# Optimization experiments

Measured on AMD Instinct MI355X. Metric: run time of the kernel, lower is better.

Reference implementation:

```python
import jax, jax.numpy as jnp
import numpy as np

B, S, D, H, W1, G = 2, 4096, 768, 12, 256, 8  # W1 = one-sided window (attention_window // 2)
HD = D // H
NC = S // W1  # number of query chunks of size W1
NEG = -1e9


def setup_inputs():
    key = jax.random.key(0)
    ks = jax.random.split(key, 9)
    def w(k):
        return jax.random.normal(k, (D, D), jnp.float32) * 0.02
    zb = jnp.zeros((D,), jnp.float32)
    # mask: >0 global, 0 local, <0 masked. First G tokens are global.
    mask = jnp.zeros((B, 1, 1, S), jnp.int32).at[:, :, :, :G].set(1)
    return {
        "hidden_states": jax.random.normal(ks[0], (B, S, D), jnp.float32),
        "attention_mask": mask,
        "Wq": w(ks[1]), "bq": zb,
        "Wk": w(ks[2]), "bk": zb,
        "Wv": w(ks[3]), "bv": zb,
        "Wqg": w(ks[4]), "bqg": zb,
        "Wkg": w(ks[5]), "bkg": zb,
        "Wvg": w(ks[6]), "bvg": zb,
        "Wo": w(ks[7]), "bo": zb,
        "n_global": G,
    }


def reference(hidden_states, attention_mask, Wq, bq, Wk, bk, Wv, bv,
              Wqg, bqg, Wkg, bkg, Wvg, bvg, Wo, bo, n_global):
    g = n_global
    mask = attention_mask.reshape(B, S)
    key_neg = mask < 0  # masked-out positions
    scale = 1.0 / np.sqrt(HD)

    def heads(x):  # [B,S,D] -> [B,H,S,HD]
        return x.reshape(B, S, H, HD).transpose(0, 2, 1, 3)

    q = heads(hidden_states @ Wq + bq) * scale
    k = heads(hidden_states @ Wk + bk)
    v = heads(hidden_states @ Wv + bv)

    # ---- sliding-window (banded) scores via 3-chunk gather ----
    idx = jnp.arange(NC)[:, None] * W1 + jnp.arange(3 * W1)[None, :]  # [NC,3W] into padded seq
    k_ch = jnp.pad(k, ((0, 0), (0, 0), (W1, W1), (0, 0)))[:, :, idx]  # [B,H,NC,3W,HD]
    q_ch = q.reshape(B, H, NC, W1, HD)
    band = jnp.einsum('bhcqd,bhckd->bhcqk', q_ch, k_ch)  # [B,H,NC,W,3W]

    qi = jnp.arange(W1)
    kj = jnp.arange(3 * W1)
    band_ok = jnp.abs(kj[None, :] - W1 - qi[:, None]) <= W1        # [W,3W] |j-i|<=w
    j_abs = idx - W1                                               # absolute key index
    in_range = (j_abs >= 0) & (j_abs < S)                          # [NC,3W]
    neg_ch = jnp.pad(key_neg, ((0, 0), (W1, W1)))[:, idx]          # [B,NC,3W]
    valid = (band_ok[None, None, None]
             & in_range[None, None, :, None, :]
             & (~neg_ch)[:, None, :, None, :])                     # [B,1,NC,W,3W]
    band = jnp.where(valid, band, NEG)

    # ---- scores of every query against the global keys (regular k proj) ----
    glob = jnp.einsum('bhsd,bhgd->bhsg', q, k[:, :, :g])           # [B,H,S,G]
    glob = jnp.where(key_neg[:, None, None, :g], NEG, glob)

    scores = jnp.concatenate([glob.reshape(B, H, NC, W1, g), band], axis=-1)
    probs = jax.nn.softmax(scores, axis=-1)
    probs = jnp.where(key_neg.reshape(B, 1, NC, W1, 1), 0.0, probs)  # zero masked query rows

    v_ch = jnp.pad(v, ((0, 0), (0, 0), (W1, W1), (0, 0)))[:, :, idx]
    out = jnp.einsum('bhcqk,bhckd->bhcqd', probs[..., g:], v_ch)
    out = out + jnp.einsum('bhcqg,bhgd->bhcqd', probs[..., :g], v[:, :, :g])
    out = out.reshape(B, H, S, HD)

    # ---- global tokens: full attention with dedicated global projections ----
    qg = heads(hidden_states @ Wqg + bqg)[:, :, :g] * scale        # [B,H,G,HD]
    kg = heads(hidden_states @ Wkg + bkg)
    vg = heads(hidden_states @ Wvg + bvg)
    gs = jnp.einsum('bhgd,bhsd->bhgs', qg, kg)                     # [B,H,G,S]
    gs = jnp.where(key_neg[:, None, None, :], NEG, gs)
    gp = jax.nn.softmax(gs, axis=-1)
    og = jnp.einsum('bhgs,bhsd->bhgd', gp, vg)
    out = out.at[:, :, :g].set(og)

    merged = out.transpose(0, 2, 1, 3).reshape(B, S, D)
    return merged @ Wo + bo  # outer output projection
```

## Files before the change

### kernel.cpp

```cpp
#include <hip/hip_runtime.h>

#define BB 2
#define SS 4096
#define DD 768
#define HH 12
#define HDD 64
#define W1C 256
#define NCC 16
#define GG 8

typedef unsigned short u16;
typedef __attribute__((ext_vector_type(4))) unsigned short u16x4;
typedef __attribute__((ext_vector_type(8))) unsigned short u16x8;
typedef __attribute__((ext_vector_type(8))) short s16x8;
typedef __attribute__((ext_vector_type(4))) float f32x4;

__device__ __forceinline__ float b2f(u16 u) {
  union { unsigned int i; float f; } v;
  v.i = ((unsigned int)u) << 16;
  return v.f;
}
__device__ __forceinline__ u16 f2b(float f) {
  union { float f; unsigned int i; } v;
  v.f = f;
  unsigned int r = v.i + 0x7FFFu + ((v.i >> 16) & 1u);
  return (u16)(r >> 16);
}
__device__ __forceinline__ float fexp2(float x) {
#if __has_builtin(__builtin_amdgcn_exp2f)
  return __builtin_amdgcn_exp2f(x);
#else
  return exp2f(x);
#endif
}
__device__ __forceinline__ unsigned pk_bf16(float lo, float hi) {
  unsigned r;
  asm("v_cvt_pk_bf16_f32 %0, %1, %2" : "=v"(r) : "v"(lo), "v"(hi));
  return r;
}
__device__ __forceinline__ void load_lds16(const void* g, void* l) {
  __builtin_amdgcn_global_load_lds(
      (const __attribute__((address_space(1))) unsigned int*)g,
      (__attribute__((address_space(3))) unsigned int*)l, 16, 0, 0);
}

#define QSCALE 0.18033688011112042f

struct WtArgs { const float* W[6]; };

__global__ __launch_bounds__(256) void prep(
    const float* __restrict__ hs, WtArgs wa, const float* __restrict__ Wqg,
    const float* __restrict__ bqg, u16* __restrict__ Ab,
    u16* __restrict__ WT, u16* __restrict__ QG) {
  __shared__ __align__(16) char pshm[24576];
  const int bid = blockIdx.x;
  const int t = threadIdx.x;

  if (bid < 3072) {
    int i = bid * 256 + t;
    const float4* p = (const float4*)(hs + (size_t)i * 8);
    float4 a = p[0], b = p[1];
    u16x8 o;
    o[0] = f2b(a.x); o[1] = f2b(a.y); o[2] = f2b(a.z); o[3] = f2b(a.w);
    o[4] = f2b(b.x); o[5] = f2b(b.y); o[6] = f2b(b.z); o[7] = f2b(b.w);
    *(u16x8*)(Ab + (size_t)i * 8) = o;
  } else if (bid < 3936) {
    float (*T)[65] = (float (*)[65])pshm;
    const int t2 = bid - 3072;
    const int mat = t2 / 144;
    const int rem = t2 % 144;
    const int k0 = (rem / 12) * 64;
    const int n0 = (rem % 12) * 64;
    const float* __restrict__ W = wa.W[mat];
#pragma unroll
    for (int i = 0; i < 4; i++) {
      int idx4 = t + i * 256;
      int r = idx4 >> 4, c4 = idx4 & 15;
      float4 v = *(const float4*)(W + (size_t)(k0 + r) * 768 + n0 + c4 * 4);
      T[r][c4 * 4 + 0] = v.x; T[r][c4 * 4 + 1] = v.y;
      T[r][c4 * 4 + 2] = v.z; T[r][c4 * 4 + 3] = v.w;
    }
    __syncthreads();
#pragma unroll
    for (int i = 0; i < 2; i++) {
      int ci = t + i * 256;
      int nl = ci >> 3, k8 = ci & 7;
      u16x8 o;
#pragma unroll
      for (int jj = 0; jj < 8; jj++) o[jj] = f2b(T[k8 * 8 + jj][nl]);
      *(u16x8*)(WT + ((size_t)mat * 768 + n0 + nl) * 768 + k0 + k8 * 8) = o;
    }
  } else {
    float (*hsL)[768] = (float (*)[768])pshm;
    const int bh = bid - 3936;
    const int b = bh / HH, h = bh % HH;
#pragma unroll
    for (int i = 0; i < 6; i++) {
      int idx = t + i * 256;
      int row = idx / 192, c4 = idx % 192;
      *(float4*)&hsL[row][c4 * 4] =
          *(const float4*)(hs + ((size_t)b * SS + row) * DD + c4 * 4);
    }
    __syncthreads();
#pragma unroll
    for (int rep = 0; rep < 2; rep++) {
      int qi = rep * 4 + (t >> 6);
      int d = t & 63, n = h * 64 + d;
      float acc = bqg[n];
      for (int k = 0; k < DD; k++)
        acc = fmaf(hsL[qi][k], Wqg[(size_t)k * DD + n], acc);
      QG[((size_t)bh * 16 + qi) * 64 + d] = f2b(acc * QSCALE);
    }
#pragma unroll
    for (int i = 0; i < 2; i++) {
      int idx = t + i * 256;
      int row = 8 + (idx >> 6), d = idx & 63;
      QG[((size_t)bh * 16 + row) * 64 + d] = 0;
    }
  }
}

struct BiasArgs { const float* bias[5]; };

template <int MODE>
__global__ __launch_bounds__(512, 1) void gemm_bf16(
    const u16* __restrict__ A, const u16* __restrict__ WT, BiasArgs ba,
    u16* __restrict__ outb, float* __restrict__ outf) {
  constexpr int NTL = (MODE == 0) ? 15 : 3;
  constexpr int NWG = 64 * NTL;
  constexpr int NT = 12;
  constexpr int ABYTES = 128 * 64 * 2;
  constexpr int BBYTES = 256 * 64 * 2;
  constexpr int BUFB = ABYTES + BBYTES;

  extern __shared__ __align__(16) char smem[];

  const int tid = threadIdx.x;
  const int w = tid >> 6, l = tid & 63;
  const int lq = l & 15, g = l >> 4;
  const int wm = w >> 2, wn = w & 3;

  const int cpx = NWG >> 3;
  const int id = (int)blockIdx.x;
  const int swz = (id & 7) * cpx + (id >> 3);
  const int bm = swz / NTL, bn = swz % NTL;
  const int m0 = bm * 128;
  const int nw0 = bn * 256;
  const int wsel = (MODE == 0) ? (bn / 3) : 0;
  const int nmat0 = (MODE == 0) ? ((bn % 3) * 256) : (bn * 256);
  const float* __restrict__ bias = ba.bias[wsel];

  f32x4 acc[4][4];
#pragma unroll
  for (int i = 0; i < 4; i++)
#pragma unroll
    for (int j = 0; j < 4; j++) acc[i][j] = (f32x4){0.f, 0.f, 0.f, 0.f};

  auto stage = [&](int t) {
    const int k0 = t * 64;
    char* uA = smem + (t % 3) * BUFB;
    char* uB = uA + ABYTES;
#pragma unroll
    for (int j = 0; j < 2; j++) {
      const int ci = j * 8 + w;
      const int p = ci * 64 + l;
      const int row = p >> 3, sl = p & 7;
      load_lds16(A + (size_t)(m0 + row) * 768 + k0 + ((sl ^ (row & 7)) * 8),
                 uA + ci * 1024);
    }
#pragma unroll
    for (int j = 0; j < 4; j++) {
      const int ci = j * 8 + w;
      const int p = ci * 64 + l;
      const int row = p >> 3, sl = p & 7;
      load_lds16(WT + (size_t)(nw0 + row) * 768 + k0 + ((sl ^ (row & 7)) * 8),
                 uB + ci * 1024);
    }
  };

  stage(0);
  stage(1);
  asm volatile("s_waitcnt vmcnt(6)" ::: "memory");
  __builtin_amdgcn_sched_barrier(0);
  __builtin_amdgcn_s_barrier();
  __builtin_amdgcn_sched_barrier(0);

  for (int kt = 0; kt < NT; kt++) {
    const u16* rA = (const u16*)(smem + (kt % 3) * BUFB);
    const u16* rB = (const u16*)(smem + (kt % 3) * BUFB + ABYTES);

    if (kt < NT - 2) stage(kt + 2);
    __builtin_amdgcn_sched_barrier(0);

    s16x8 af[4][2], bf[4][2];
#pragma unroll
    for (int mi = 0; mi < 4; mi++) {
      const int r = wm * 64 + mi * 16 + lq;
#pragma unroll
      for (int ks = 0; ks < 2; ks++)
        af[mi][ks] =
            *(const s16x8*)(rA + r * 64 + (((ks * 4 + g) ^ (r & 7)) * 8));
    }
#pragma unroll
    for (int nj = 0; nj < 4; nj++) {
      const int r = wn * 64 + nj * 16 + lq;
#pragma unroll
      for (int ks = 0; ks < 2; ks++)
        bf[nj][ks] =
            *(const s16x8*)(rB + r * 64 + (((ks * 4 + g) ^ (r & 7)) * 8));
    }
#pragma unroll
    for (int mi = 0; mi < 4; mi++)
#pragma unroll
      for (int nj = 0; nj < 4; nj++)
#pragma unroll
        for (int ks = 0; ks < 2; ks++)
          acc[mi][nj] = __builtin_amdgcn_mfma_f32_16x16x32_bf16(
              af[mi][ks], bf[nj][ks], acc[mi][nj], 0, 0, 0);

    if (kt < NT - 2)
      asm volatile("s_waitcnt vmcnt(6)" ::: "memory");
    else
      asm volatile("s_waitcnt vmcnt(0)" ::: "memory");
    __builtin_amdgcn_sched_barrier(0);
    __builtin_amdgcn_s_barrier();
    __builtin_amdgcn_sched_barrier(0);
  }

  if (MODE == 0) {
    const float scale = (wsel == 0) ? QSCALE : 1.0f;
    u16* outw = outb + (size_t)wsel * ((size_t)BB * HH * SS * HDD);
#pragma unroll
    for (int nj = 0; nj < 4; nj++) {
      const int c = nmat0 + wn * 64 + nj * 16 + lq;
      const float bv = bias[c];
      const int h = c >> 6, hd = c & 63;
#pragma unroll
      for (int mi = 0; mi < 4; mi++) {
#pragma unroll
        for (int r = 0; r < 4; r++) {
          const int m = m0 + wm * 64 + mi * 16 + g * 4 + r;
          const int b = m >> 12, s = m & 4095;
          outw[((size_t)(b * HH + h) * SS + s) * HDD + hd] =
              f2b((acc[mi][nj][r] + bv) * scale);
        }
      }
    }
  } else {
#pragma unroll
    for (int nj = 0; nj < 4; nj++) {
      const int c = nmat0 + wn * 64 + nj * 16 + lq;
      const float bv = bias[c];
#pragma unroll
      for (int mi = 0; mi < 4; mi++) {
#pragma unroll
        for (int r = 0; r < 4; r++) {
          const int m = m0 + wm * 64 + mi * 16 + g * 4 + r;
          outf[(size_t)m * 768 + c] = acc[mi][nj][r] + bv;
        }
      }
    }
  }
}

__global__ __launch_bounds__(512, 4) void attn_band(
    const u16* __restrict__ Q, const u16* __restrict__ K,
    const u16* __restrict__ V, const int* __restrict__ amask,
    u16* __restrict__ ATT) {
  __shared__ __align__(16) char smem[32768];
  const int tid = threadIdx.x;
  const int w = tid >> 6, lane = tid & 63;
  const int lq = lane & 15, g = lane >> 4;
  const int h = blockIdx.y, b = blockIdx.z;
  const int bh = b * HH + h;
  const size_t bhs = (size_t)bh * SS;
  const int q0 = (int)blockIdx.x * 128;

  s16x8 qf[2];
  {
    const u16* qp = Q + (bhs + q0 + w * 16 + lq) * 64;
    qf[0] = *(const s16x8*)(qp + g * 8);
    qf[1] = *(const s16x8*)(qp + 32 + g * 8);
  }

  f32x4 oacc[4];
#pragma unroll
  for (int i = 0; i < 4; i++) oacc[i] = (f32x4){0.f, 0.f, 0.f, 0.f};
  float denom = 0.f;

  const int NT = 11;
  u16x8 vreg;

  auto jof = [&](int t) { return t < 10 ? q0 - 256 + t * 64 : 0; };

  auto stage_issue = [&](int t) {
    const int j0 = jof(t);
    char* Kb_ = smem + (t & 1) * 16384;
    const int row = tid >> 3, sl = tid & 7;
    if (j0 >= 0 && j0 + 64 <= SS) {
      load_lds16(K + (bhs + j0 + row) * 64 + ((sl ^ (row & 7)) * 8),
                 Kb_ + w * 1024);
    } else {
      int jj = j0 + row;
      u16x8 val;
#pragma unroll
      for (int e = 0; e < 8; e++) val[e] = 0;
      if ((unsigned)jj < (unsigned)SS)
        val = *(const u16x8*)(K + (bhs + jj) * 64 + ((sl ^ (row & 7)) * 8));
      *(u16x8*)(Kb_ + tid * 16) = val;
    }
    int jj = j0 + lane;
    u16x8 vv;
#pragma unroll
    for (int e = 0; e < 8; e++) vv[e] = 0;
    if ((unsigned)jj < (unsigned)SS)
      vv = *(const u16x8*)(V + (bhs + jj) * 64 + w * 8);
    vreg = vv;
  };

  stage_issue(0);

  for (int kt = 0; kt < NT; kt++) {
    const int j0 = jof(kt);
    const int cur = kt & 1;
    char* Kl = smem + cur * 16384;
    char* VT = Kl + 8192;
    const bool bandfree = (kt == 10);
    const int klimit = bandfree ? 8 : 64;

    int jm = j0 + lane;
    int mv = ((unsigned)jm < (unsigned)SS) ? amask[b * SS + jm] : -1;
    bool okk = (mv >= 0) && (lane < klimit);
    unsigned long long vm = __ballot(okk);

    asm volatile("s_waitcnt vmcnt(0)" ::: "memory");
#pragma unroll
    for (int e = 0; e < 8; e++)
      *(u16*)(VT + (w * 8 + e) * 128 + ((lane * 2) ^ (e << 4))) = vreg[e];
    asm volatile("s_waitcnt lgkmcnt(0)" ::: "memory");
    __builtin_amdgcn_sched_barrier(0);
    __builtin_amdgcn_s_barrier();
    __builtin_amdgcn_sched_barrier(0);

    if (kt + 1 < NT) stage_issue(kt + 1);

    f32x4 sc[4];
#pragma unroll
    for (int i = 0; i < 4; i++) sc[i] = (f32x4){0.f, 0.f, 0.f, 0.f};
#pragma unroll
    for (int s = 0; s < 2; s++) {
#pragma unroll
      for (int ks = 0; ks < 4; ks++) {
        s16x8 kf = *(const s16x8*)(Kl + (ks * 16 + lq) * 128 +
                                   (((s * 4 + g) ^ (lq & 7)) << 4));
        sc[ks] = __builtin_amdgcn_mfma_f32_16x16x32_bf16(kf, qf[s], sc[ks],
                                                          0, 0, 0);
      }
    }

    {
      const unsigned mlo = (unsigned)vm, mhi = (unsigned)(vm >> 32);
      const int q_abs = q0 + w * 16 + lq;
      const int qw = q0 + w * 16;
      const bool allin = bandfree || (j0 >= qw - 241 && j0 <= qw + 193);
      const bool fast = (vm == ~0ull) && allin;
      const int ddq = j0 + g * 4 - q_abs;
      const int gsh = g * 4;
      if (fast) {
#pragma unroll
        for (int ks = 0; ks < 4; ks++)
#pragma unroll
          for (int r = 0; r < 4; r++) {
            float p = fexp2(sc[ks][r]);
            sc[ks][r] = p;
            denom += p;
          }
      } else {
#pragma unroll
        for (int ks = 0; ks < 4; ks++)
#pragma unroll
          for (int r = 0; r < 4; r++) {
            float e = fexp2(sc[ks][r]);
            unsigned bit =
                ((ks < 2 ? mlo : mhi) >> (gsh + ((ks & 1) * 16 + r))) & 1u;
            bool ok = bit && (allin ||
                              (unsigned)(ddq + ks * 16 + r + 256) <= 512u);
            float p = ok ? e : 0.f;
            sc[ks][r] = p;
            denom += p;
          }
      }
    }

#pragma unroll
    for (int s = 0; s < 2; s++) {
      const int srcA = lq + ((g & 1) << 5);
      const bool hiSel = g >= 2;
      float L[4], H[4];
#pragma unroll
      for (int r = 0; r < 4; r++) {
        float a0 = __shfl(sc[2 * s][r], srcA);
        float a1 = __shfl(sc[2 * s + 1][r], srcA);
        L[r] = hiSel ? a1 : a0;
        float b0 = __shfl(sc[2 * s][r], srcA + 16);
        float b1 = __shfl(sc[2 * s + 1][r], srcA + 16);
        H[r] = hiSel ? b1 : b0;
      }
      union { unsigned u[4]; s16x8 v; } pf;
      pf.u[0] = pk_bf16(L[0], L[1]);
      pf.u[1] = pk_bf16(L[2], L[3]);
      pf.u[2] = pk_bf16(H[0], H[1]);
      pf.u[3] = pk_bf16(H[2], H[3]);
#pragma unroll
      for (int dblk = 0; dblk < 4; dblk++) {
        s16x8 vf = *(const s16x8*)(VT + (dblk * 16 + lq) * 128 +
                                   (((s * 4 + g) ^ (lq & 7)) << 4));
        oacc[dblk] = __builtin_amdgcn_mfma_f32_16x16x32_bf16(vf, pf.v,
                                                              oacc[dblk],
                                                              0, 0, 0);
      }
    }

    __builtin_amdgcn_sched_barrier(0);
    __builtin_amdgcn_s_barrier();
    __builtin_amdgcn_sched_barrier(0);
  }

  denom += __shfl_xor(denom, 16);
  denom += __shfl_xor(denom, 32);
  const int q_abs = q0 + w * 16 + lq;
  const float rowscale = (amask[b * SS + q_abs] >= 0) ? (1.f / denom) : 0.f;
  u16* orow = ATT + ((size_t)b * SS + q_abs) * DD + h * 64;
#pragma unroll
  for (int dblk = 0; dblk < 4; dblk++) {
    u16x4 o;
#pragma unroll
    for (int r = 0; r < 4; r++) o[r] = f2b(oacc[dblk][r] * rowscale);
    *(u16x4*)(orow + dblk * 16 + g * 4) = o;
  }
}

__global__ __launch_bounds__(256) void attn_global(
    const u16* __restrict__ Q, const u16* __restrict__ K,
    const u16* __restrict__ V, const int* __restrict__ amask,
    float* __restrict__ Pnum, float* __restrict__ Pden) {
  extern __shared__ __align__(16) char smem[];
  const int tid = threadIdx.x;
  const int w = tid >> 6, lane = tid & 63;
  const int lq = lane & 15, g = lane >> 4;
  const int h = blockIdx.y, b = blockIdx.z;
  const int bh = b * HH + h;
  const size_t bhs = (size_t)bh * SS;
  const int split = (int)blockIdx.x;

  char* Kl = smem + w * 16384;
  char* VT = Kl + 8192;

  s16x8 qf[2];
  {
    const u16* qp = Q + ((size_t)bh * 16 + lq) * 64;
    qf[0] = *(const s16x8*)(qp + g * 8);
    qf[1] = *(const s16x8*)(qp + 32 + g * 8);
  }

  f32x4 oacc[4];
#pragma unroll
  for (int i = 0; i < 4; i++) oacc[i] = (f32x4){0.f, 0.f, 0.f, 0.f};
  float denom = 0.f;

  for (int kt = 0; kt < 2; kt++) {
    const int j0 = split * 512 + (w * 2 + kt) * 64;

    int jm = j0 + lane;
    int mv = amask[b * SS + jm];
    unsigned long long vm = __ballot(mv >= 0);

    asm volatile("s_waitcnt lgkmcnt(0)" ::: "memory");
    const u16* Ks = K + bhs * 64 + (size_t)j0 * 64;
#pragma unroll
    for (int i = 0; i < 8; i++) {
      int ci = i * 64 + lane;
      int row = ci >> 3, cc = ci & 7, cs = cc ^ (row & 7);
      load_lds16(Ks + row * 64 + cs * 8, Kl + i * 1024);
    }
    const u16* Vs = V + bhs * 64 + (size_t)j0 * 64;
#pragma unroll
    for (int p = 0; p < 8; p++) {
      u16x8 vv = *(const u16x8*)(Vs + (size_t)lane * 64 + p * 8);
#pragma unroll
      for (int e = 0; e < 8; e++)
        *(u16*)(VT + (p * 8 + e) * 128 + ((lane * 2) ^ (e << 4))) = vv[e];
    }
    asm volatile("s_waitcnt vmcnt(0) lgkmcnt(0)" ::: "memory");

    f32x4 sc[4];
#pragma unroll
    for (int i = 0; i < 4; i++) sc[i] = (f32x4){0.f, 0.f, 0.f, 0.f};
#pragma unroll
    for (int s = 0; s < 2; s++) {
#pragma unroll
      for (int ks = 0; ks < 4; ks++) {
        s16x8 kf = *(const s16x8*)(Kl + (ks * 16 + lq) * 128 +
                                   (((s * 4 + g) ^ (lq & 7)) << 4));
        sc[ks] = __builtin_amdgcn_mfma_f32_16x16x32_bf16(kf, qf[s], sc[ks],
                                                          0, 0, 0);
      }
    }

    {
      const unsigned mlo = (unsigned)vm, mhi = (unsigned)(vm >> 32);
      const bool fast = (vm == ~0ull);
      const int gsh = g * 4;
      if (fast) {
#pragma unroll
        for (int ks = 0; ks < 4; ks++)
#pragma unroll
          for (int r = 0; r < 4; r++) {
            float p = fexp2(sc[ks][r]);
            sc[ks][r] = p;
            denom += p;
          }
      } else {
#pragma unroll
        for (int ks = 0; ks < 4; ks++)
#pragma unroll
          for (int r = 0; r < 4; r++) {
            float e = fexp2(sc[ks][r]);
            unsigned bit =
                ((ks < 2 ? mlo : mhi) >> (gsh + ((ks & 1) * 16 + r))) & 1u;
            float p = bit ? e : 0.f;
            sc[ks][r] = p;
            denom += p;
          }
      }
    }

#pragma unroll
    for (int s = 0; s < 2; s++) {
      const int srcA = lq + ((g & 1) << 5);
      const bool hiSel = g >= 2;
      float L[4], H[4];
#pragma unroll
      for (int r = 0; r < 4; r++) {
        float a0 = __shfl(sc[2 * s][r], srcA);
        float a1 = __shfl(sc[2 * s + 1][r], srcA);
        L[r] = hiSel ? a1 : a0;
        float b0 = __shfl(sc[2 * s][r], srcA + 16);
        float b1 = __shfl(sc[2 * s + 1][r], srcA + 16);
        H[r] = hiSel ? b1 : b0;
      }
      union { unsigned u[4]; s16x8 v; } pf;
      pf.u[0] = pk_bf16(L[0], L[1]);
      pf.u[1] = pk_bf16(L[2], L[3]);
      pf.u[2] = pk_bf16(H[0], H[1]);
      pf.u[3] = pk_bf16(H[2], H[3]);
#pragma unroll
      for (int dblk = 0; dblk < 4; dblk++) {
        s16x8 vf = *(const s16x8*)(VT + (dblk * 16 + lq) * 128 +
                                   (((s * 4 + g) ^ (lq & 7)) << 4));
        oacc[dblk] = __builtin_amdgcn_mfma_f32_16x16x32_bf16(vf, pf.v,
                                                              oacc[dblk],
                                                              0, 0, 0);
      }
    }
  }

  denom += __shfl_xor(denom, 16);
  denom += __shfl_xor(denom, 32);
  const int pidx = split * 4 + w;
  float* np = Pnum + ((size_t)bh * 32 + pidx) * 1024;
#pragma unroll
  for (int dblk = 0; dblk < 4; dblk++)
#pragma unroll
    for (int r = 0; r < 4; r++)
      np[(dblk * 16 + g * 4 + r) * 16 + lq] = oacc[dblk][r];
  Pden[((size_t)bh * 32 + pidx) * 16 + lq] = denom;
}

__global__ __launch_bounds__(512) void gmerge(const float* __restrict__ Pnum,
                                              const float* __restrict__ Pden,
                                              u16* __restrict__ ATT) {
  const int bh = blockIdx.x;
  const int b = bh / HH, h = bh % HH;
  const int t = threadIdx.x;
  const int q = t >> 6, d = t & 63;
  float num = 0.f, den = 0.f;
#pragma unroll 4
  for (int p = 0; p < 32; p++) {
    num += Pnum[((size_t)bh * 32 + p) * 1024 + d * 16 + q];
    den += Pden[((size_t)bh * 32 + p) * 16 + q];
  }
  ATT[((size_t)b * SS + q) * DD + h * 64 + d] = f2b(num / den);
}

extern "C" void kernel_launch(void* const* d_in, const int* in_sizes, int n_in,
                              void* d_out, int out_size, void* d_ws,
                              size_t ws_size, hipStream_t stream) {
  const float* hs = (const float*)d_in[0];
  const int* amask = (const int*)d_in[1];
  const float* Wq = (const float*)d_in[2];
  const float* bq = (const float*)d_in[3];
  const float* Wk = (const float*)d_in[4];
  const float* bk = (const float*)d_in[5];
  const float* Wv = (const float*)d_in[6];
  const float* bv = (const float*)d_in[7];
  const float* Wqg = (const float*)d_in[8];
  const float* bqg = (const float*)d_in[9];
  const float* Wkg = (const float*)d_in[10];
  const float* bkg = (const float*)d_in[11];
  const float* Wvg = (const float*)d_in[12];
  const float* bvg = (const float*)d_in[13];
  const float* Wo = (const float*)d_in[14];
  const float* bo = (const float*)d_in[15];
  float* out = (float*)d_out;

  char* ws = (char*)d_ws;
  const size_t QSZB = (size_t)BB * HH * SS * HDD * 2;
  u16* Qb = (u16*)(ws + 0);
  u16* Kb = (u16*)(ws + QSZB);
  u16* Vb = (u16*)(ws + 2 * QSZB);
  u16* KGb = (u16*)(ws + 3 * QSZB);
  u16* VGb = (u16*)(ws + 4 * QSZB);
  u16* Ab = (u16*)(ws + 5 * QSZB);
  u16* WTb = (u16*)(ws + 6 * QSZB);
  u16* ATTb = (u16*)(ws + 6 * QSZB + 7077888);
  u16* QGb = (u16*)(ws + 7 * QSZB + 7077888);
  float* Pnum = (float*)(ws + 7 * QSZB + 7077888 + 49152);
  float* Pden = (float*)(ws + 7 * QSZB + 7077888 + 49152 + 3145728);

  WtArgs wa;
  wa.W[0] = Wq; wa.W[1] = Wk; wa.W[2] = Wv;
  wa.W[3] = Wkg; wa.W[4] = Wvg; wa.W[5] = Wo;
  hipLaunchKernelGGL(prep, dim3(3960), dim3(256), 0, stream, hs, wa, Wqg,
                     bqg, Ab, WTb, QGb);

  BiasArgs b0;
  b0.bias[0] = bq; b0.bias[1] = bk; b0.bias[2] = bv;
  b0.bias[3] = bkg; b0.bias[4] = bvg;
  hipLaunchKernelGGL((gemm_bf16<0>), dim3(960), dim3(512), 147456, stream,
                     Ab, WTb, b0, Qb, (float*)nullptr);

  hipLaunchKernelGGL(attn_global, dim3(8, HH, BB), dim3(256), 65536, stream,
                     QGb, KGb, VGb, amask, Pnum, Pden);

  hipLaunchKernelGGL(attn_band, dim3(32, HH, BB), dim3(512), 0, stream, Qb,
                     Kb, Vb, amask, ATTb);

  hipLaunchKernelGGL(gmerge, dim3(24), dim3(512), 0, stream, Pnum, Pden, ATTb);

  BiasArgs b1;
  for (int i = 0; i < 5; i++) b1.bias[i] = bo;
  hipLaunchKernelGGL((gemm_bf16<1>), dim3(192), dim3(512), 147456, stream,
                     ATTb, WTb + (size_t)5 * 768 * 768, b1, (u16*)nullptr,
                     out);
}
```

Before: 198.1 us.

## Replace QKV projection GEMM with 256x256-tile, phase-interleaved ping-pong kernel

```diff
diff --git a/kernel.cpp b/kernel.cpp
--- a/kernel.cpp
+++ b/kernel.cpp
@@ -121,6 +121,134 @@
 }
 
 struct BiasArgs { const float* bias[5]; };
+
+__global__ __launch_bounds__(512, 1) void gemm0_8p(
+    const u16* __restrict__ A, const u16* __restrict__ WT, BiasArgs ba,
+    u16* __restrict__ outb) {
+  constexpr int NTL = 15;
+  constexpr int NWG = 480;
+  constexpr int NT = 12;
+  constexpr int TBYTES = 256 * 64 * 2;
+  constexpr int BUFB = 2 * TBYTES;
+
+  extern __shared__ __align__(16) char smem[];
+
+  const int tid = threadIdx.x;
+  const int w = tid >> 6, l = tid & 63;
+  const int lq = l & 15, g = l >> 4;
+  const int wm = w >> 2, wn = w & 3;
+
+  const int cpx = NWG >> 3;
+  const int id = (int)blockIdx.x;
+  const int swz = (id & 7) * cpx + (id >> 3);
+  const int bm = swz / NTL, bn = swz % NTL;
+  const int m0 = bm * 256;
+  const int nw0 = bn * 256;
+  const int wsel = bn / 3;
+  const int nmat0 = (bn % 3) * 256;
+  const float* __restrict__ bias = ba.bias[wsel];
+
+  f32x4 acc[8][4];
+#pragma unroll
+  for (int i = 0; i < 8; i++)
+#pragma unroll
+    for (int j = 0; j < 4; j++) acc[i][j] = (f32x4){0.f, 0.f, 0.f, 0.f};
+
+  auto stageH = [&](int t, int mat, int h) {
+    const int k0 = t * 64;
+    char* dst = smem + (t & 1) * BUFB + mat * TBYTES + h * 16384;
+    const u16* src = mat ? WT : A;
+    const int rbase = (mat ? nw0 : m0) + h * 128;
+#pragma unroll
+    for (int j = 0; j < 2; j++) {
+      const int p = (j * 8 + w) * 64 + l;
+      const int row = p >> 3, sl = p & 7;
+      load_lds16(src + (size_t)(rbase + row) * 768 + k0 +
+                     ((sl ^ (row & 7)) * 8),
+                 dst + (j * 8 + w) * 1024);
+    }
+  };
+
+  stageH(0, 0, 0); stageH(0, 0, 1); stageH(0, 1, 0); stageH(0, 1, 1);
+  stageH(1, 0, 0);
+  asm volatile("s_waitcnt vmcnt(2)" ::: "memory");
+  __builtin_amdgcn_sched_barrier(0);
+  __builtin_amdgcn_s_barrier();
+  __builtin_amdgcn_sched_barrier(0);
+
+  s16x8 bf[4];
+
+  for (int kt = 0; kt < NT; kt++) {
+    const u16* rA = (const u16*)(smem + (kt & 1) * BUFB);
+    const u16* rB = (const u16*)(smem + (kt & 1) * BUFB + TBYTES);
+
+#pragma unroll
+    for (int ph = 0; ph < 4; ph++) {
+      const int mh = ph & 1;
+      const int kh = ph >> 1;
+      s16x8 af[4];
+#pragma unroll
+      for (int mi = 0; mi < 4; mi++) {
+        const int r = wm * 128 + (mh * 4 + mi) * 16 + lq;
+        af[mi] =
+            *(const s16x8*)(rA + r * 64 + (((kh * 4 + g) ^ (r & 7)) * 8));
+      }
+      if (mh == 0) {
+#pragma unroll
+        for (int nj = 0; nj < 4; nj++) {
+          const int r = wn * 64 + nj * 16 + lq;
+          bf[nj] =
+              *(const s16x8*)(rB + r * 64 + (((kh * 4 + g) ^ (r & 7)) * 8));
+        }
+      }
+      if (ph == 0) { if (kt + 1 < NT) stageH(kt + 1, 0, 1); }
+      else if (ph == 1) { if (kt + 1 < NT) stageH(kt + 1, 1, 0); }
+      else if (ph == 2) { if (kt + 1 < NT) stageH(kt + 1, 1, 1); }
+      else { if (kt + 2 < NT) stageH(kt + 2, 0, 0); }
+
+      __builtin_amdgcn_s_barrier();
+      asm volatile("s_waitcnt lgkmcnt(0)" ::: "memory");
+      __builtin_amdgcn_sched_barrier(0);
+      __builtin_amdgcn_s_setprio(1);
+#pragma unroll
+      for (int mi = 0; mi < 4; mi++)
+#pragma unroll
+        for (int nj = 0; nj < 4; nj++)
+          acc[mh * 4 + mi][nj] = __builtin_amdgcn_mfma_f32_16x16x32_bf16(
+              af[mi], bf[nj], acc[mh * 4 + mi][nj], 0, 0, 0);
+      __builtin_amdgcn_s_setprio(0);
+
+      if (ph == 3) {
+        if (kt < NT - 2)
+          asm volatile("s_waitcnt vmcnt(2)" ::: "memory");
+        else
+          asm volatile("s_waitcnt vmcnt(0)" ::: "memory");
+      }
+      __builtin_amdgcn_sched_barrier(0);
+      __builtin_amdgcn_s_barrier();
+      __builtin_amdgcn_sched_barrier(0);
+    }
+  }
+
+  const float scale = (wsel == 0) ? QSCALE : 1.0f;
+  u16* outw = outb + (size_t)wsel * ((size_t)BB * HH * SS * HDD);
+#pragma unroll
+  for (int nj = 0; nj < 4; nj++) {
+    const int c = nmat0 + wn * 64 + nj * 16 + lq;
+    const float bv = bias[c];
+    const int h = c >> 6, hd = c & 63;
+#pragma unroll
+    for (int mi = 0; mi < 8; mi++) {
+#pragma unroll
+      for (int r = 0; r < 4; r++) {
+        const int m = m0 + wm * 128 + mi * 16 + g * 4 + r;
+        const int b = m >> 12, s = m & 4095;
+        outw[((size_t)(b * HH + h) * SS + s) * HDD + hd] =
+            f2b((acc[mi][nj][r] + bv) * scale);
+      }
+    }
+  }
+}
 
 template <int MODE>
 __global__ __launch_bounds__(512, 1) void gemm_bf16(
@@ -637,8 +765,8 @@
   BiasArgs b0;
   b0.bias[0] = bq; b0.bias[1] = bk; b0.bias[2] = bv;
   b0.bias[3] = bkg; b0.bias[4] = bvg;
-  hipLaunchKernelGGL((gemm_bf16<0>), dim3(960), dim3(512), 147456, stream,
-                     Ab, WTb, b0, Qb, (float*)nullptr);
+  hipLaunchKernelGGL(gemm0_8p, dim3(480), dim3(512), 131072, stream, Ab,
+                     WTb, b0, Qb);
 
   hipLaunchKernelGGL(attn_global, dim3(8, HH, BB), dim3(256), 65536, stream,
                      QGb, KGb, VGb, amask, Pnum, Pden);
```

Result: faster. 194.2 us (-2.0%).
